# Kernel optimization log

Hardware: AMD Instinct MI355X
Metric: run time of the kernel (lower is better)

Reference implementation:

```python
import jax, jax.numpy as jnp
import numpy as np

IN_FEATURES = 512
OUT_FEATURES = 256
N = 2048

def setup_inputs() -> dict:
    key = jax.random.key(0)
    k1, k2, k3 = jax.random.split(key, 3)
    x = jax.random.normal(k1, (N, IN_FEATURES), dtype=jnp.float32)
    # kaiming_uniform_(a=sqrt(5)) -> uniform(-b, b) with b = sqrt(6/((1+5)*fan_in)) = 1/sqrt(fan_in)
    bound_w = 1.0 / np.sqrt(IN_FEATURES)
    weight = jax.random.uniform(k2, (OUT_FEATURES, IN_FEATURES), dtype=jnp.float32,
                                minval=-bound_w, maxval=bound_w)
    bound_b = 1.0 / np.sqrt(IN_FEATURES)
    bias = jax.random.uniform(k3, (OUT_FEATURES,), dtype=jnp.float32,
                              minval=-bound_b, maxval=bound_b)
    return {"x": x, "weight": weight, "bias": bias}

def reference(x, weight, bias):
    # MAM fully-connected (beta == 0 path):
    # prod[n, k, j] = x[n, k] * weight[j, k]
    # C[n, j] = max_k prod[n,k,j] + min_k prod[n,k,j] + bias[j]
    prod = x[:, :, None] * weight.T[None, :, :]   # [N, in, out]
    C = jnp.max(prod, axis=1) + jnp.min(prod, axis=1) + bias[None, :]
    return C
```

## Files before the change

### kernel.cpp

```cpp
#include <hip/hip_runtime.h>
#include <math.h>

#define N_ 2048
#define K_ 512
#define J_ 256

typedef float f32x4 __attribute__((ext_vector_type(4)));
typedef __attribute__((address_space(3))) float       lds_f;
typedef const __attribute__((address_space(1))) float glb_f;

#define MAX3(acc, a, b) asm("v_max3_f32 %0, %0, %1, %2" : "+v"(acc) : "v"(a), "v"(b))
#define MIN3(acc, a, b) asm("v_min3_f32 %0, %0, %1, %2" : "+v"(acc) : "v"(a), "v"(b))

__global__ __launch_bounds__(512, 2) void mam_fused11(
    const float* __restrict__ x, const float* __restrict__ w,
    const float* __restrict__ bias, float* __restrict__ out)
{
    __shared__ __align__(16) float sm[24576];

    const int t    = threadIdx.x;
    const int lane = t & 63;
    const int kq   = __builtin_amdgcn_readfirstlane(t >> 6);

    const int wg0 = (int)blockIdx.x;
    const int wg  = (wg0 & 7) * 32 + (wg0 >> 3);
    const int bx  = wg & 7;
    const int by  = wg >> 3;
    const int n0  = by * 64;
    const int j0  = bx * 32;

    const int rn = lane >> 3;
    const int cj = lane & 7;

    float mx[8][4], mn[8][4];
#pragma unroll
    for (int i = 0; i < 8; ++i)
#pragma unroll
        for (int jj = 0; jj < 4; ++jj) {
            mx[i][jj] = -__builtin_inff();
            mn[i][jj] =  __builtin_inff();
        }

#define STAGE(buf, s)                                                          \
    {                                                                          \
        const int kb = (s) * 128;                                              \
        _Pragma("unroll")                                                      \
        for (int u = 0; u < 4; ++u) {             \
            const int li  = kq * 4 + u;                                        \
            const int row = 2 * li + (lane >> 5);                              \
            __builtin_amdgcn_global_load_lds(                                  \
                (glb_f*)(x + (size_t)(n0 + row) * K_ + kb                      \
                         + (((lane & 31) ^ (row & 7)) << 2)),                  \
                (lds_f*)(sm + (buf) * 8192 + li * 256), 16, 0, 0);             \
        }                                                                      \
        _Pragma("unroll")                                                      \
        for (int u = 0; u < 2; ++u) {             \
            const int wi  = kq * 2 + u;                                        \
            const int col = 2 * wi + (lane >> 5);                              \
            __builtin_amdgcn_global_load_lds(                                  \
                (glb_f*)(w + (size_t)(j0 + col) * K_ + kb                      \
                         + (((lane & 31) ^ (col & 7)) << 2)),                  \
                (lds_f*)(sm + 16384 + (buf) * 4096 + wi * 256), 16, 0, 0);     \
        }                                                                      \
    }

    f32x4 AXv[8], AWv[4], BXv[8], BWv[4];

#define READQ(Xv, Wv, xa, wa, WCNT)                                            \
    asm volatile(                                                              \
        "ds_read_b128 %0, %12\n\t"                                             \
        "ds_read_b128 %1, %12 offset:4096\n\t"                                 \
        "ds_read_b128 %2, %12 offset:8192\n\t"                                 \
        "ds_read_b128 %3, %12 offset:12288\n\t"                                \
        "ds_read_b128 %4, %12 offset:16384\n\t"                                \
        "ds_read_b128 %5, %12 offset:20480\n\t"                                \
        "ds_read_b128 %6, %12 offset:24576\n\t"                                \
        "ds_read_b128 %7, %12 offset:28672\n\t"                                \
        "ds_read_b128 %8, %13\n\t"                                             \
        "ds_read_b128 %9, %13 offset:4096\n\t"                                 \
        "ds_read_b128 %10, %13 offset:8192\n\t"                                \
        "ds_read_b128 %11, %13 offset:12288\n\t"                               \
        WCNT                                                                   \
        : "=&v"(Xv[0]), "=&v"(Xv[1]), "=&v"(Xv[2]), "=&v"(Xv[3]),              \
          "=&v"(Xv[4]), "=&v"(Xv[5]), "=&v"(Xv[6]), "=&v"(Xv[7]),              \
          "=&v"(Wv[0]), "=&v"(Wv[1]), "=&v"(Wv[2]), "=&v"(Wv[3])               \
        : "v"(xa), "v"(wa));                                                   \
    __builtin_amdgcn_sched_barrier(0);

#define COMPQ(Xv, Wv)                                                          \
    _Pragma("unroll")                                                          \
    for (int i = 0; i < 8; ++i)                                                \
        _Pragma("unroll")                                                      \
        for (int jj = 0; jj < 4; ++jj) {                                       \
            const f32x4 a = Xv[i], b = Wv[jj];                                 \
            const float p0 = a.x * b.x, p1 = a.y * b.y;                        \
            const float p2 = a.z * b.z, p3 = a.w * b.w;                        \
            MAX3(mx[i][jj], p0, p1); MAX3(mx[i][jj], p2, p3);                  \
            MIN3(mn[i][jj], p0, p1); MIN3(mn[i][jj], p2, p3);                  \
        }

#define COMP(buf)                                                              \
    {                                                                          \
        const unsigned xb0 = (buf) * 32768u + (unsigned)(rn * 512);            \
        const unsigned wb0 = 65536u + (buf) * 16384u + (unsigned)(cj * 512);   \
        const unsigned xa0 = xb0 + (unsigned)((((kq * 4 + 0) ^ rn)) << 4);     \
        const unsigned wa0 = wb0 + (unsigned)((((kq * 4 + 0) ^ cj)) << 4);     \
        const unsigned xa1 = xb0 + (unsigned)((((kq * 4 + 1) ^ rn)) << 4);     \
        const unsigned wa1 = wb0 + (unsigned)((((kq * 4 + 1) ^ cj)) << 4);     \
        const unsigned xa2 = xb0 + (unsigned)((((kq * 4 + 2) ^ rn)) << 4);     \
        const unsigned wa2 = wb0 + (unsigned)((((kq * 4 + 2) ^ cj)) << 4);     \
        const unsigned xa3 = xb0 + (unsigned)((((kq * 4 + 3) ^ rn)) << 4);     \
        const unsigned wa3 = wb0 + (unsigned)((((kq * 4 + 3) ^ cj)) << 4);     \
        READQ(AXv, AWv, xa0, wa0, "");                                         \
        READQ(BXv, BWv, xa1, wa1, "s_waitcnt lgkmcnt(12)\n\t");                \
        COMPQ(AXv, AWv);                                                       \
        READQ(AXv, AWv, xa2, wa2, "s_waitcnt lgkmcnt(12)\n\t");                \
        COMPQ(BXv, BWv);                                                       \
        READQ(BXv, BWv, xa3, wa3, "s_waitcnt lgkmcnt(12)\n\t");                \
        COMPQ(AXv, AWv);                                                       \
        asm volatile("s_waitcnt lgkmcnt(0)");                                  \
        __builtin_amdgcn_sched_barrier(0);                                     \
        COMPQ(BXv, BWv);                                                       \
    }

    STAGE(0, 0);
    __syncthreads();
    STAGE(1, 1);  COMP(0);
    __syncthreads();
    STAGE(0, 2);  COMP(1);
    __syncthreads();
    STAGE(1, 3);  COMP(0);
    __syncthreads();
                  COMP(1);
    __syncthreads();

#undef STAGE
#undef READQ
#undef COMPQ
#undef COMP

    float2* cb = (float2*)sm;
#pragma unroll
    for (int h = 0; h < 2; ++h) {
#pragma unroll
        for (int i = 0; i < 8; ++i)
#pragma unroll
            for (int jh = 0; jh < 2; ++jh) {
                const int jj = 2 * h + jh;
                float2 v; v.x = mx[i][jj]; v.y = mn[i][jj];
                cb[(kq * 64 + rn + 8 * i) * 17 + cj + 8 * jh] = v;
            }
        __syncthreads();
#pragma unroll
        for (int e = 0; e < 2; ++e) {
            const int o   = t + e * 512;
            const int row = o >> 4;
            const int c16 = o & 15;
            float a = -__builtin_inff(), b = __builtin_inff();
#pragma unroll
            for (int c = 0; c < 8; ++c) {
                const float2 v = cb[(c * 64 + row) * 17 + c16];
                a = fmaxf(a, v.x);
                b = fminf(b, v.y);
            }
            const int j = j0 + 16 * h + c16;
            out[(size_t)(n0 + row) * J_ + j] = a + b + bias[j];
        }
        __syncthreads();
    }
}

extern "C" void kernel_launch(void* const* d_in, const int* in_sizes, int n_in,
                              void* d_out, int out_size, void* d_ws, size_t ws_size,
                              hipStream_t stream) {
    const float* x    = (const float*)d_in[0];
    const float* w    = (const float*)d_in[1];
    const float* bias = (const float*)d_in[2];
    float* out = (float*)d_out;

    dim3 grid(256);
    mam_fused11<<<grid, 512, 0, stream>>>(x, w, bias, out);
}
```

Before: 71.54 us.

## Halve per-block row tile to 32 and double grid with higher occupancy

Shrinks each workgroup's N tile from 64 to 32 rows, so the grid doubles to 512 blocks. LDS use drops to 64 KB and launch bounds target 4 blocks per CU. Per-thread accumulators and register buffers shrink, and the products are now written as 2-wide vector multiplies that could map to packed FP32 ops. The aim is better occupancy and CU coverage on a chip with many CUs. The cost is that each W tile is reused across fewer rows, so W loads and staging overhead per output element go up.

```diff
diff --git a/kernel.cpp b/kernel.cpp
--- a/kernel.cpp
+++ b/kernel.cpp
@@ -6,35 +6,36 @@
 #define J_ 256
 
 typedef float f32x4 __attribute__((ext_vector_type(4)));
+typedef float f32x2 __attribute__((ext_vector_type(2)));
 typedef __attribute__((address_space(3))) float       lds_f;
 typedef const __attribute__((address_space(1))) float glb_f;
 
 #define MAX3(acc, a, b) asm("v_max3_f32 %0, %0, %1, %2" : "+v"(acc) : "v"(a), "v"(b))
 #define MIN3(acc, a, b) asm("v_min3_f32 %0, %0, %1, %2" : "+v"(acc) : "v"(a), "v"(b))
 
-__global__ __launch_bounds__(512, 2) void mam_fused11(
+__global__ __launch_bounds__(512, 4) void mam_fused12(
     const float* __restrict__ x, const float* __restrict__ w,
     const float* __restrict__ bias, float* __restrict__ out)
 {
-    __shared__ __align__(16) float sm[24576];
+    __shared__ __align__(16) float sm[16384];
 
     const int t    = threadIdx.x;
     const int lane = t & 63;
     const int kq   = __builtin_amdgcn_readfirstlane(t >> 6);
 
     const int wg0 = (int)blockIdx.x;
-    const int wg  = (wg0 & 7) * 32 + (wg0 >> 3);
+    const int wg  = (wg0 & 7) * 64 + (wg0 >> 3);
     const int bx  = wg & 7;
     const int by  = wg >> 3;
-    const int n0  = by * 64;
+    const int n0  = by * 32;
     const int j0  = bx * 32;
 
     const int rn = lane >> 3;
     const int cj = lane & 7;
 
-    float mx[8][4], mn[8][4];
+    float mx[4][4], mn[4][4];
 #pragma unroll
-    for (int i = 0; i < 8; ++i)
+    for (int i = 0; i < 4; ++i)
 #pragma unroll
         for (int jj = 0; jj < 4; ++jj) {
             mx[i][jj] = -__builtin_inff();
@@ -45,64 +46,58 @@
     {                                                                          \
         const int kb = (s) * 128;                                              \
         _Pragma("unroll")                                                      \
-        for (int u = 0; u < 4; ++u) {             \
-            const int li  = kq * 4 + u;                                        \
+        for (int u = 0; u < 2; ++u) {             \
+            const int li  = kq * 2 + u;                                        \
             const int row = 2 * li + (lane >> 5);                              \
             __builtin_amdgcn_global_load_lds(                                  \
                 (glb_f*)(x + (size_t)(n0 + row) * K_ + kb                      \
                          + (((lane & 31) ^ (row & 7)) << 2)),                  \
-                (lds_f*)(sm + (buf) * 8192 + li * 256), 16, 0, 0);             \
+                (lds_f*)(sm + (buf) * 4096 + li * 256), 16, 0, 0);             \
         }                                                                      \
         _Pragma("unroll")                                                      \
         for (int u = 0; u < 2; ++u) {             \
-            const int wi  = kq * 2 + u;                                        \
-            const int col = 2 * wi + (lane >> 5);                              \
+            const int li  = kq * 2 + u;                                        \
+            const int col = 2 * li + (lane >> 5);                              \
             __builtin_amdgcn_global_load_lds(                                  \
                 (glb_f*)(w + (size_t)(j0 + col) * K_ + kb                      \
                          + (((lane & 31) ^ (col & 7)) << 2)),                  \
-                (lds_f*)(sm + 16384 + (buf) * 4096 + wi * 256), 16, 0, 0);     \
+                (lds_f*)(sm + 8192 + (buf) * 4096 + li * 256), 16, 0, 0);      \
         }                                                                      \
     }
 
-    f32x4 AXv[8], AWv[4], BXv[8], BWv[4];
+    f32x4 AX[4], AW[4], BX[4], BW[4];
 
 #define READQ(Xv, Wv, xa, wa, WCNT)                                            \
     asm volatile(                                                              \
-        "ds_read_b128 %0, %12\n\t"                                             \
-        "ds_read_b128 %1, %12 offset:4096\n\t"                                 \
-        "ds_read_b128 %2, %12 offset:8192\n\t"                                 \
-        "ds_read_b128 %3, %12 offset:12288\n\t"                                \
-        "ds_read_b128 %4, %12 offset:16384\n\t"                                \
-        "ds_read_b128 %5, %12 offset:20480\n\t"                                \
-        "ds_read_b128 %6, %12 offset:24576\n\t"                                \
-        "ds_read_b128 %7, %12 offset:28672\n\t"                                \
-        "ds_read_b128 %8, %13\n\t"                                             \
-        "ds_read_b128 %9, %13 offset:4096\n\t"                                 \
-        "ds_read_b128 %10, %13 offset:8192\n\t"                                \
-        "ds_read_b128 %11, %13 offset:12288\n\t"                               \
+        "ds_read_b128 %0, %8\n\t"                                              \
+        "ds_read_b128 %1, %8 offset:4096\n\t"                                  \
+        "ds_read_b128 %2, %8 offset:8192\n\t"                                  \
+        "ds_read_b128 %3, %8 offset:12288\n\t"                                 \
+        "ds_read_b128 %4, %9\n\t"                                              \
+        "ds_read_b128 %5, %9 offset:4096\n\t"                                  \
+        "ds_read_b128 %6, %9 offset:8192\n\t"                                  \
+        "ds_read_b128 %7, %9 offset:12288\n\t"                                 \
         WCNT                                                                   \
         : "=&v"(Xv[0]), "=&v"(Xv[1]), "=&v"(Xv[2]), "=&v"(Xv[3]),              \
-          "=&v"(Xv[4]), "=&v"(Xv[5]), "=&v"(Xv[6]), "=&v"(Xv[7]),              \
           "=&v"(Wv[0]), "=&v"(Wv[1]), "=&v"(Wv[2]), "=&v"(Wv[3])               \
         : "v"(xa), "v"(wa));                                                   \
     __builtin_amdgcn_sched_barrier(0);
 
 #define COMPQ(Xv, Wv)                                                          \
     _Pragma("unroll")                                                          \
-    for (int i = 0; i < 8; ++i)                                                \
+    for (int i = 0; i < 4; ++i)                                                \
         _Pragma("unroll")                                                      \
         for (int jj = 0; jj < 4; ++jj) {                                       \
-            const f32x4 a = Xv[i], b = Wv[jj];                                 \
-            const float p0 = a.x * b.x, p1 = a.y * b.y;                        \
-            const float p2 = a.z * b.z, p3 = a.w * b.w;                        \
-            MAX3(mx[i][jj], p0, p1); MAX3(mx[i][jj], p2, p3);                  \
-            MIN3(mn[i][jj], p0, p1); MIN3(mn[i][jj], p2, p3);                  \
+            const f32x2 plo = Xv[i].lo * Wv[jj].lo;                            \
+            const f32x2 phi = Xv[i].hi * Wv[jj].hi;                            \
+            MAX3(mx[i][jj], plo.x, plo.y); MAX3(mx[i][jj], phi.x, phi.y);      \
+            MIN3(mn[i][jj], plo.x, plo.y); MIN3(mn[i][jj], phi.x, phi.y);      \
         }
 
 #define COMP(buf)                                                              \
     {                                                                          \
-        const unsigned xb0 = (buf) * 32768u + (unsigned)(rn * 512);            \
-        const unsigned wb0 = 65536u + (buf) * 16384u + (unsigned)(cj * 512);   \
+        const unsigned xb0 = (buf) * 16384u + (unsigned)(rn * 512);            \
+        const unsigned wb0 = 32768u + (buf) * 16384u + (unsigned)(cj * 512);   \
         const unsigned xa0 = xb0 + (unsigned)((((kq * 4 + 0) ^ rn)) << 4);     \
         const unsigned wa0 = wb0 + (unsigned)((((kq * 4 + 0) ^ cj)) << 4);     \
         const unsigned xa1 = xb0 + (unsigned)((((kq * 4 + 1) ^ rn)) << 4);     \
@@ -111,16 +106,16 @@
         const unsigned wa2 = wb0 + (unsigned)((((kq * 4 + 2) ^ cj)) << 4);     \
         const unsigned xa3 = xb0 + (unsigned)((((kq * 4 + 3) ^ rn)) << 4);     \
         const unsigned wa3 = wb0 + (unsigned)((((kq * 4 + 3) ^ cj)) << 4);     \
-        READQ(AXv, AWv, xa0, wa0, "");                                         \
-        READQ(BXv, BWv, xa1, wa1, "s_waitcnt lgkmcnt(12)\n\t");                \
-        COMPQ(AXv, AWv);                                                       \
-        READQ(AXv, AWv, xa2, wa2, "s_waitcnt lgkmcnt(12)\n\t");                \
-        COMPQ(BXv, BWv);                                                       \
-        READQ(BXv, BWv, xa3, wa3, "s_waitcnt lgkmcnt(12)\n\t");                \
-        COMPQ(AXv, AWv);                                                       \
+        READQ(AX, AW, xa0, wa0, "");                                           \
+        READQ(BX, BW, xa1, wa1, "s_waitcnt lgkmcnt(8)\n\t");                   \
+        COMPQ(AX, AW);                                                         \
+        READQ(AX, AW, xa2, wa2, "s_waitcnt lgkmcnt(8)\n\t");                   \
+        COMPQ(BX, BW);                                                         \
+        READQ(BX, BW, xa3, wa3, "s_waitcnt lgkmcnt(8)\n\t");                   \
+        COMPQ(AX, AW);                                                         \
         asm volatile("s_waitcnt lgkmcnt(0)");                                  \
         __builtin_amdgcn_sched_barrier(0);                                     \
-        COMPQ(BXv, BWv);                                                       \
+        COMPQ(BX, BW);                                                         \
     }
 
     STAGE(0, 0);
@@ -143,23 +138,21 @@
 #pragma unroll
     for (int h = 0; h < 2; ++h) {
 #pragma unroll
-        for (int i = 0; i < 8; ++i)
+        for (int i = 0; i < 4; ++i)
 #pragma unroll
             for (int jh = 0; jh < 2; ++jh) {
                 const int jj = 2 * h + jh;
                 float2 v; v.x = mx[i][jj]; v.y = mn[i][jj];
-                cb[(kq * 64 + rn + 8 * i) * 17 + cj + 8 * jh] = v;
+                cb[(kq * 32 + rn + 8 * i) * 17 + cj + 8 * jh] = v;
             }
         __syncthreads();
-#pragma unroll
-        for (int e = 0; e < 2; ++e) {
-            const int o   = t + e * 512;
-            const int row = o >> 4;
-            const int c16 = o & 15;
+        {
+            const int row = t >> 4;
+            const int c16 = t & 15;
             float a = -__builtin_inff(), b = __builtin_inff();
 #pragma unroll
             for (int c = 0; c < 8; ++c) {
-                const float2 v = cb[(c * 64 + row) * 17 + c16];
+                const float2 v = cb[(c * 32 + row) * 17 + c16];
                 a = fmaxf(a, v.x);
                 b = fminf(b, v.y);
             }
@@ -178,6 +171,6 @@
     const float* bias = (const float*)d_in[2];
     float* out = (float*)d_out;
 
-    dim3 grid(256);
-    mam_fused11<<<grid, 512, 0, stream>>>(x, w, bias, out);
+    dim3 grid(512);
+    mam_fused12<<<grid, 512, 0, stream>>>(x, w, bias, out);
 }
```

Measured after the change: 72.74 us. About the same (+1.7%).
